# Optimization experiments

Hardware: AMD Instinct MI355X
Metric: run time of the kernel (lower is better)

## Reference

```python
import jax, jax.numpy as jnp
import numpy as np

EMBED_DIM = 512
NUM_HEADS = 8
HEAD_DIM = EMBED_DIM // NUM_HEADS


def setup_inputs() -> dict:
    key = jax.random.key(0)
    k_x, k_qkv, k_proj, k_pb = jax.random.split(key, 4)
    B, N, C = 2, 4096, EMBED_DIM
    x = jax.random.normal(k_x, (B, N, C), dtype=jnp.float32)
    # nn.Linear(embed_dim, 3*embed_dim, bias=False): weight [3C, C], y = x @ W.T
    s = 1.0 / np.sqrt(C)
    w_qkv = jax.random.uniform(k_qkv, (3 * C, C), dtype=jnp.float32, minval=-s, maxval=s)
    w_proj = jax.random.uniform(k_proj, (C, C), dtype=jnp.float32, minval=-s, maxval=s)
    b_proj = jax.random.uniform(k_pb, (C,), dtype=jnp.float32, minval=-s, maxval=s)
    return {"x": x, "w_qkv": w_qkv, "w_proj": w_proj, "b_proj": b_proj}


def reference(x, w_qkv, w_proj, b_proj):
    B, N, C = x.shape
    H, D = NUM_HEADS, HEAD_DIM
    scale = D ** -0.5
    qkv = jnp.einsum('bnc,fc->bnf', x, w_qkv)           # [B, N, 3C]
    qkv = qkv.reshape(B, N, 3, H, D)
    q, k, v = [jnp.transpose(qkv[:, :, i], (0, 2, 1, 3)) for i in range(3)]  # [B,H,N,D]
    attn = jnp.einsum('bhnd,bhmd->bhnm', q, k) * scale  # [B,H,N,N]
    # additive causal mask: -inf above the diagonal
    causal = jnp.triu(jnp.full((N, N), -jnp.inf, dtype=attn.dtype), k=1)
    attn = jax.nn.softmax(attn + causal, axis=-1)
    out = jnp.einsum('bhnm,bhmd->bhnd', attn, v)        # [B,H,N,D]
    out = jnp.transpose(out, (0, 2, 1, 3)).reshape(B, N, C)
    return jnp.einsum('bnc,oc->bno', out, w_proj) + b_proj
```

## Files before the change

kernel.cpp:

```cpp
#include <hip/hip_runtime.h>
#include <hip/hip_bf16.h>


typedef __attribute__((ext_vector_type(8))) short s16x8;
typedef __attribute__((ext_vector_type(4))) float f32x4;

#define QSCALE 0.18033688011112042f

__device__ __forceinline__ ushort f2bf(float f) {
  unsigned u = __float_as_uint(f);
  u = (u + 0x7FFFu + ((u >> 16) & 1u)) >> 16;
  return (ushort)u;
}

__device__ __forceinline__ unsigned cvt_pk_bf16(float a, float b) {
  unsigned r;
  asm("v_cvt_pk_bf16_f32 %0, %1, %2" : "=v"(r) : "v"(a), "v"(b));
  return r;
}

__device__ __forceinline__ float bflo(unsigned u) { return __uint_as_float(u << 16); }
__device__ __forceinline__ float bfhi(unsigned u) { return __uint_as_float(u & 0xffff0000u); }

__global__ __launch_bounds__(256) void cvt_all(const float* __restrict__ x,
                                               const float* __restrict__ wq,
                                               const float* __restrict__ wp,
                                               ushort* __restrict__ xb,
                                               ushort* __restrict__ wqb,
                                               ushort* __restrict__ wpb) {
  int i = blockIdx.x * 256 + threadIdx.x;
  const float* src;
  ushort* dst;
  int off;
  if (i < 1048576) {
    src = x; dst = xb; off = i;
  } else if (i < 1245184) {
    src = wq; dst = wqb; off = i - 1048576;
  } else {
    src = wp; dst = wpb; off = i - 1245184;
  }
  float4 v = reinterpret_cast<const float4*>(src)[off];
  ushort4 o;
  o.x = f2bf(v.x); o.y = f2bf(v.y); o.z = f2bf(v.z); o.w = f2bf(v.w);
  reinterpret_cast<ushort4*>(dst)[off] = o;
}

template <int EPI>
__global__ __launch_bounds__(256) void gemm_bt(const ushort* __restrict__ A,
                                               const ushort* __restrict__ W,
                                               ushort* __restrict__ q_ws,
                                               ushort* __restrict__ k_ws,
                                               ushort* __restrict__ vt_ws,
                                               float* __restrict__ outf,
                                               const float* __restrict__ bias) {
  __shared__ ushort As[128 * 32];
  __shared__ ushort Bs[128 * 32];
  const int tid = threadIdx.x;
  const int lane = tid & 63, wv = tid >> 6;
  const int wm = wv >> 1, wn = wv & 1;
  const int l15 = lane & 15, g = lane >> 4;
  const int tm = blockIdx.y * 128, tn = blockIdx.x * 128;

  f32x4 acc[4][4] = {};

  for (int k0 = 0; k0 < 512; k0 += 32) {
#pragma unroll
    for (int it = 0; it < 2; ++it) {
      int slot = it * 256 + tid;
      int row = slot >> 2;
      int ch = (slot & 3) ^ ((row >> 1) & 3);
      const int sb = (it * 256 + wv * 64) * 8;
      __builtin_amdgcn_global_load_lds(
          (const __attribute__((address_space(1))) void*)(A + (size_t)(tm + row) * 512 + k0 +
                                                          ch * 8),
          (__attribute__((address_space(3))) void*)(As + sb), 16, 0, 0);
      __builtin_amdgcn_global_load_lds(
          (const __attribute__((address_space(1))) void*)(W + (size_t)(tn + row) * 512 + k0 +
                                                          ch * 8),
          (__attribute__((address_space(3))) void*)(Bs + sb), 16, 0, 0);
    }
    __syncthreads();
    s16x8 af[4], bfr[4];
#pragma unroll
    for (int i = 0; i < 4; ++i) {
      int Ra = wm * 64 + i * 16 + l15;
      af[i] = reinterpret_cast<const s16x8*>(As)[Ra * 4 + (g ^ ((Ra >> 1) & 3))];
      int Rb = wn * 64 + i * 16 + l15;
      bfr[i] = reinterpret_cast<const s16x8*>(Bs)[Rb * 4 + (g ^ ((Rb >> 1) & 3))];
    }
#pragma unroll
    for (int mi = 0; mi < 4; ++mi)
#pragma unroll
      for (int ni = 0; ni < 4; ++ni)
        acc[mi][ni] =
            __builtin_amdgcn_mfma_f32_16x16x32_bf16(af[mi], bfr[ni], acc[mi][ni], 0, 0, 0);
    __syncthreads();
  }

  const int rowb = tm + wm * 64 + g * 4;
  const int colb = tn + wn * 64 + l15;
#pragma unroll
  for (int mi = 0; mi < 4; ++mi) {
#pragma unroll
    for (int ni = 0; ni < 4; ++ni) {
      int r0 = rowb + mi * 16;
      int col = colb + ni * 16;
      if (EPI == 0) {
        int i3 = col >> 9, h = (col >> 6) & 7, d = col & 63;
        int b = r0 >> 12;
        int bh = b * 8 + h;
        if (i3 == 2) {
          int n0 = r0 & 4095;
          int kt = n0 >> 6, ce = (n0 >> 5) & 1, ge = (n0 >> 3) & 3, je = n0 & 7;
          int nbe = d >> 4, le = d & 15;
          ushort4 pk;
          pk.x = f2bf(acc[mi][ni][0]);
          pk.y = f2bf(acc[mi][ni][1]);
          pk.z = f2bf(acc[mi][ni][2]);
          pk.w = f2bf(acc[mi][ni][3]);
          *reinterpret_cast<ushort4*>(
              vt_ws + (((size_t)bh * 64 + kt) * 8 + nbe * 2 + ce) * 512 + (ge * 16 + le) * 8 +
              je) = pk;
        } else if (i3 == 1) {
          int ce = d >> 5, ge = (d >> 3) & 3, je = d & 7;
#pragma unroll
          for (int r = 0; r < 4; ++r) {
            int n = (r0 + r) & 4095;
            int kt = n >> 6, le = n & 15, nbe = (n >> 4) & 3;
            k_ws[(((size_t)bh * 64 + kt) * 8 + nbe * 2 + ce) * 512 + (ge * 16 + le) * 8 + je] =
                f2bf(acc[mi][ni][r]);
          }
        } else {
          int n0 = r0 & 4095;
#pragma unroll
          for (int r = 0; r < 4; ++r)
            q_ws[((size_t)bh * 4096 + (n0 + r)) * 64 + d] = f2bf(acc[mi][ni][r] * QSCALE);
        }
      } else {
#pragma unroll
        for (int r = 0; r < 4; ++r)
          outf[(size_t)(r0 + r) * 512 + col] = acc[mi][ni][r] + bias[col];
      }
    }
  }
}

__global__ __launch_bounds__(64, 2) void attn_kernel(const ushort* __restrict__ Q,
                                                     const ushort* __restrict__ Kk,
                                                     const ushort* __restrict__ Vt,
                                                     ushort* __restrict__ O,
                                                     ushort* __restrict__ po,
                                                     float* __restrict__ ml) {
  __shared__ ushort P_lds[32 * 64];
  const int lane = threadIdx.x & 63;
  const int l15 = lane & 15, g = lane >> 4;
  const int L = blockIdx.x;
  const int p = L & 7, j2 = L >> 3;
  const int bh = p * 2 + (j2 & 1);
  const int i = j2 >> 1;
  const int r = i / 3;
  const int kind = i - r * 3;
  int qt, klo, khi, half = 0;
  bool partial;
  if (kind == 2) {
    qt = 63 - r;
    partial = false;
    klo = 0;
    khi = qt >> 1;
  } else {
    qt = 127 - r;
    partial = true;
    half = kind;
    const int ktm = qt >> 1;
    const int mid = (ktm + 2) >> 1;
    klo = kind ? mid : 0;
    khi = kind ? ktm : (mid - 1);
  }
  const int ktmax = qt >> 1;
  const int qw = qt * 32;
  const size_t baseQ = (size_t)bh * 4096 * 64;

  s16x8 aq[2][2];
#pragma unroll
  for (int s = 0; s < 2; ++s) {
    const ushort* qp = Q + baseQ + (size_t)(qw + s * 16 + l15) * 64 + g * 8;
    aq[s][0] = *reinterpret_cast<const s16x8*>(qp);
    aq[s][1] = *reinterpret_cast<const s16x8*>(qp + 32);
  }

  f32x4 o[2][4] = {};
  float m[2] = {-1e30f, -1e30f};
  float l[2] = {0.f, 0.f};
  const int swz = (l15 & 7) << 3;
  const ushort* kb = Kk + ((size_t)bh * 64) * 4096 + lane * 8;
  const ushort* vb = Vt + ((size_t)bh * 64) * 4096 + lane * 8;

  s16x8 kfA[8], kfB[8];
#pragma unroll
  for (int t = 0; t < 8; ++t)
    kfA[t] = *reinterpret_cast<const s16x8*>(kb + (size_t)klo * 4096 + t * 512);

#define ATTN_STEP(KC, KN, KT)                                                             \
  do {                                                                                    \
    const ushort* vp = vb + (size_t)(KT) * 4096;                                          \
    s16x8 vf[8];                                                                          \
    _Pragma("unroll") for (int t = 0; t < 8; ++t)                                         \
        vf[t] = *reinterpret_cast<const s16x8*>(vp + t * 512);                            \
    const int knx = ((KT) >= khi) ? khi : ((KT) + 1);                                     \
    const ushort* kpn = kb + (size_t)knx * 4096;                                          \
    _Pragma("unroll") for (int t = 0; t < 8; ++t)                                         \
        KN[t] = *reinterpret_cast<const s16x8*>(kpn + t * 512);                           \
    f32x4 st[2][4] = {};                                                                  \
    __builtin_amdgcn_s_setprio(1);                                                        \
    _Pragma("unroll") for (int nb = 0; nb < 4; ++nb) {                                    \
      _Pragma("unroll") for (int s = 0; s < 2; ++s) {                                     \
        st[s][nb] = __builtin_amdgcn_mfma_f32_16x16x32_bf16(KC[nb * 2 + 0], aq[s][0],     \
                                                            st[s][nb], 0, 0, 0);         \
        st[s][nb] = __builtin_amdgcn_mfma_f32_16x16x32_bf16(KC[nb * 2 + 1], aq[s][1],     \
                                                            st[s][nb], 0, 0, 0);         \
      }                                                                                   \
    }                                                                                     \
    __builtin_amdgcn_s_setprio(0);                                                        \
    if ((KT) == ktmax) {                                  \
      const int k0d = (KT) * 64;                                                          \
      _Pragma("unroll") for (int s = 0; s < 2; ++s)                                       \
          _Pragma("unroll") for (int nb = 0; nb < 4; ++nb)                                \
              _Pragma("unroll") for (int r2 = 0; r2 < 4; ++r2)                            \
                  if (k0d + nb * 16 + g * 4 + r2 > qw + s * 16 + l15)                     \
                    st[s][nb][r2] = -1e30f;                                               \
    }                                                                                     \
    _Pragma("unroll") for (int s = 0; s < 2; ++s) {                                       \
      float a0 = fmaxf(fmaxf(st[s][0][0], st[s][0][1]), fmaxf(st[s][0][2], st[s][0][3])); \
      float a1 = fmaxf(fmaxf(st[s][1][0], st[s][1][1]), fmaxf(st[s][1][2], st[s][1][3])); \
      float a2 = fmaxf(fmaxf(st[s][2][0], st[s][2][1]), fmaxf(st[s][2][2], st[s][2][3])); \
      float a3 = fmaxf(fmaxf(st[s][3][0], st[s][3][1]), fmaxf(st[s][3][2], st[s][3][3])); \
      float pm = fmaxf(fmaxf(a0, a1), fmaxf(a2, a3));                 \
      if (!__all(pm - m[s] <= 8.0f)) {                   \
        float pmf = fmaxf(pm, __shfl_xor(pm, 16));                                        \
        pmf = fmaxf(pmf, __shfl_xor(pmf, 32));                                            \
        const float mn = fmaxf(m[s], pmf);                                                \
        const float al = __builtin_amdgcn_exp2f(m[s] - mn);                               \
        l[s] *= al;                                                                       \
        m[s] = mn;                                                                        \
        _Pragma("unroll") for (int nb = 0; nb < 4; ++nb)                                  \
            _Pragma("unroll") for (int r2 = 0; r2 < 4; ++r2) o[s][nb][r2] *= al;          \
      }                                                                                   \
      float rs = 0.f;                                                                     \
      _Pragma("unroll") for (int nb = 0; nb < 4; ++nb) {                                  \
        float p0 = __builtin_amdgcn_exp2f(st[s][nb][0] - m[s]);                           \
        float p1 = __builtin_amdgcn_exp2f(st[s][nb][1] - m[s]);                           \
        float p2 = __builtin_amdgcn_exp2f(st[s][nb][2] - m[s]);                           \
        float p3 = __builtin_amdgcn_exp2f(st[s][nb][3] - m[s]);                           \
        rs += (p0 + p1) + (p2 + p3);                                                      \
        uint2 w;                                                                          \
        w.x = cvt_pk_bf16(p0, p1);                                                        \
        w.y = cvt_pk_bf16(p2, p3);                                                        \
        *reinterpret_cast<uint2*>(P_lds + (s * 16 + l15) * 64 +                           \
                                  ((nb * 16 + g * 4) ^ swz)) = w;                         \
      }                                                                                   \
      l[s] += rs;                                                                         \
    }                                                                                     \
    s16x8 pa[2][2];                                                                       \
    _Pragma("unroll") for (int s = 0; s < 2; ++s)                                         \
        _Pragma("unroll") for (int c = 0; c < 2; ++c)                                     \
            pa[s][c] = *reinterpret_cast<const s16x8*>(P_lds + (s * 16 + l15) * 64 +      \
                                                       ((c * 32 + g * 8) ^ swz));         \
    __builtin_amdgcn_s_setprio(1);                                                        \
    _Pragma("unroll") for (int nb = 0; nb < 4; ++nb) {                                    \
      _Pragma("unroll") for (int s = 0; s < 2; ++s) {                                     \
        o[s][nb] = __builtin_amdgcn_mfma_f32_16x16x32_bf16(vf[nb * 2 + 0], pa[s][0],      \
                                                           o[s][nb], 0, 0, 0);            \
        o[s][nb] = __builtin_amdgcn_mfma_f32_16x16x32_bf16(vf[nb * 2 + 1], pa[s][1],      \
                                                           o[s][nb], 0, 0, 0);            \
      }                                                                                   \
    }                                                                                     \
    __builtin_amdgcn_s_setprio(0);                                                        \
  } while (0)

  int kt = klo;
  for (;;) {
    ATTN_STEP(kfA, kfB, kt);
    if (++kt > khi) break;
    ATTN_STEP(kfB, kfA, kt);
    if (++kt > khi) break;
  }
#undef ATTN_STEP

  float lr[2];
#pragma unroll
  for (int s = 0; s < 2; ++s) {
    float ls = l[s];
    ls += __shfl_xor(ls, 16);
    ls += __shfl_xor(ls, 32);
    lr[s] = ls;
  }

  if (!partial) {
    const int b = bh >> 3, h = bh & 7;
#pragma unroll
    for (int s = 0; s < 2; ++s) {
      const float linv = 1.0f / lr[s];
      const size_t rowo = (size_t)(b * 4096 + qw + s * 16 + l15) * 512 + h * 64;
#pragma unroll
      for (int nb = 0; nb < 4; ++nb) {
        uint2 pk;
        pk.x = cvt_pk_bf16(o[s][nb][0] * linv, o[s][nb][1] * linv);
        pk.y = cvt_pk_bf16(o[s][nb][2] * linv, o[s][nb][3] * linv);
        *reinterpret_cast<uint2*>(&O[rowo + nb * 16 + g * 4]) = pk;
      }
    }
  } else {
    const int t2 = (bh * 64 + (qt - 64)) * 2 + half;
#pragma unroll
    for (int s = 0; s < 2; ++s) {
      const float linv = 1.0f / lr[s];
      const int row = s * 16 + l15;
      const size_t pbase = ((size_t)t2 * 32 + row) * 64;
#pragma unroll
      for (int nb = 0; nb < 4; ++nb) {
        uint2 pk;
        pk.x = cvt_pk_bf16(o[s][nb][0] * linv, o[s][nb][1] * linv);
        pk.y = cvt_pk_bf16(o[s][nb][2] * linv, o[s][nb][3] * linv);
        *reinterpret_cast<uint2*>(po + pbase + nb * 16 + g * 4) = pk;
      }
      if (g == 0) {
        float2 v;
        v.x = m[s];
        v.y = lr[s];
        *reinterpret_cast<float2*>(ml + ((size_t)t2 * 32 + row) * 2) = v;
      }
    }
  }
}

__global__ __launch_bounds__(64) void attn_merge(const ushort* __restrict__ po,
                                                 const float* __restrict__ ml,
                                                 ushort* __restrict__ O) {
  const int L = blockIdx.x, tid = threadIdx.x;
  const int p = L & 7, q2 = L >> 3;
  const int bh = p * 2 + (q2 & 1);
  const int qt = 64 + (q2 >> 1);
  const int t = bh * 64 + (qt - 64);
  const int row = tid >> 1, dh = (tid & 1) * 32;
  const float2 ml0 = *reinterpret_cast<const float2*>(ml + ((size_t)(t * 2 + 0) * 32 + row) * 2);
  const float2 ml1 = *reinterpret_cast<const float2*>(ml + ((size_t)(t * 2 + 1) * 32 + row) * 2);
  const float ms = fmaxf(ml0.x, ml1.x);
  const float w0 = __builtin_amdgcn_exp2f(ml0.x - ms) * ml0.y;
  const float w1 = __builtin_amdgcn_exp2f(ml1.x - ms) * ml1.y;
  const float inv = 1.0f / (w0 + w1);
  const float c0 = w0 * inv, c1 = w1 * inv;
  const int b = bh >> 3, h = bh & 7;
  const size_t rowo = (size_t)(b * 4096 + qt * 32 + row) * 512 + h * 64 + dh;
  const ushort* p0 = po + ((size_t)(t * 2 + 0) * 32 + row) * 64 + dh;
  const ushort* p1 = po + ((size_t)(t * 2 + 1) * 32 + row) * 64 + dh;
#pragma unroll
  for (int j = 0; j < 4; ++j) {
    uint4 a = reinterpret_cast<const uint4*>(p0)[j];
    uint4 bb = reinterpret_cast<const uint4*>(p1)[j];
    uint4 out;
    out.x = cvt_pk_bf16(c0 * bflo(a.x) + c1 * bflo(bb.x), c0 * bfhi(a.x) + c1 * bfhi(bb.x));
    out.y = cvt_pk_bf16(c0 * bflo(a.y) + c1 * bflo(bb.y), c0 * bfhi(a.y) + c1 * bfhi(bb.y));
    out.z = cvt_pk_bf16(c0 * bflo(a.z) + c1 * bflo(bb.z), c0 * bfhi(a.z) + c1 * bfhi(bb.z));
    out.w = cvt_pk_bf16(c0 * bflo(a.w) + c1 * bflo(bb.w), c0 * bfhi(a.w) + c1 * bfhi(bb.w));
    reinterpret_cast<uint4*>(&O[rowo])[j] = out;
  }
}

extern "C" void kernel_launch(void* const* d_in, const int* in_sizes, int n_in,
                              void* d_out, int out_size, void* d_ws, size_t ws_size,
                              hipStream_t stream) {
  const float* x = (const float*)d_in[0];
  const float* w_qkv = (const float*)d_in[1];
  const float* w_proj = (const float*)d_in[2];
  const float* b_proj = (const float*)d_in[3];
  float* out = (float*)d_out;

  ushort* xb = (ushort*)d_ws;
  ushort* wqkvb = xb + (size_t)8192 * 512;
  ushort* wprojb = wqkvb + (size_t)1536 * 512;
  ushort* qws = wprojb + (size_t)512 * 512;
  ushort* kws = qws + (size_t)16 * 4096 * 64;
  ushort* vtws = kws + (size_t)16 * 4096 * 64;
  ushort* ows = vtws + (size_t)16 * 4096 * 64;

  cvt_all<<<5120, 256, 0, stream>>>(x, w_qkv, w_proj, xb, wqkvb, wprojb);

  gemm_bt<0><<<dim3(12, 64), 256, 0, stream>>>(xb, wqkvb, qws, kws, vtws, nullptr, nullptr);

  ushort* po = xb;
  float* ml = (float*)wqkvb;

  attn_kernel<<<3072, 64, 0, stream>>>(qws, kws, vtws, ows, po, ml);
  attn_merge<<<1024, 64, 0, stream>>>(po, ml, ows);

  gemm_bt<1><<<dim3(4, 64), 256, 0, stream>>>(ows, wprojb, nullptr, nullptr, nullptr, out,
                                              b_proj);
}
```

Measured before the change: 116.2 us.

## Shrink attention query tile to 16 rows and double the block count

Each single-wave attention block now handles 16 query rows instead of 32. The grid, the causal split schedule and the partial-merge indexing are rescaled so the number of blocks doubles, and launch bounds now ask for 3 waves per SIMD. The goal is more parallelism and occupancy through fewer registers per wave. In exchange, every K/V tile is loaded from memory twice as often per query row, since each loaded tile now feeds half as many MFMAs.

```diff
diff --git a/kernel.cpp b/kernel.cpp
--- a/kernel.cpp
+++ b/kernel.cpp
@@ -145,13 +145,13 @@
   }
 }
 
-__global__ __launch_bounds__(64, 2) void attn_kernel(const ushort* __restrict__ Q,
+__global__ __launch_bounds__(64, 3) void attn_kernel(const ushort* __restrict__ Q,
                                                      const ushort* __restrict__ Kk,
                                                      const ushort* __restrict__ Vt,
                                                      ushort* __restrict__ O,
                                                      ushort* __restrict__ po,
                                                      float* __restrict__ ml) {
-  __shared__ ushort P_lds[32 * 64];
+  __shared__ ushort P_lds[16 * 64];
   const int lane = threadIdx.x & 63;
   const int l15 = lane & 15, g = lane >> 4;
   const int L = blockIdx.x;
@@ -163,34 +163,33 @@
   int qt, klo, khi, half = 0;
   bool partial;
   if (kind == 2) {
-    qt = 63 - r;
+    qt = 127 - r;
     partial = false;
     klo = 0;
-    khi = qt >> 1;
+    khi = qt >> 2;
   } else {
-    qt = 127 - r;
+    qt = 255 - r;
     partial = true;
     half = kind;
-    const int ktm = qt >> 1;
+    const int ktm = qt >> 2;
     const int mid = (ktm + 2) >> 1;
     klo = kind ? mid : 0;
     khi = kind ? ktm : (mid - 1);
   }
-  const int ktmax = qt >> 1;
-  const int qw = qt * 32;
+  const int ktmax = qt >> 2;
+  const int qw = qt * 16;
   const size_t baseQ = (size_t)bh * 4096 * 64;
 
-  s16x8 aq[2][2];
-#pragma unroll
-  for (int s = 0; s < 2; ++s) {
-    const ushort* qp = Q + baseQ + (size_t)(qw + s * 16 + l15) * 64 + g * 8;
-    aq[s][0] = *reinterpret_cast<const s16x8*>(qp);
-    aq[s][1] = *reinterpret_cast<const s16x8*>(qp + 32);
-  }
-
-  f32x4 o[2][4] = {};
-  float m[2] = {-1e30f, -1e30f};
-  float l[2] = {0.f, 0.f};
+  s16x8 aq0, aq1;
+  {
+    const ushort* qp = Q + baseQ + (size_t)(qw + l15) * 64 + g * 8;
+    aq0 = *reinterpret_cast<const s16x8*>(qp);
+    aq1 = *reinterpret_cast<const s16x8*>(qp + 32);
+  }
+
+  f32x4 o[4] = {};
+  float m = -1e30f;
+  float l = 0.f;
   const int swz = (l15 & 7) << 3;
   const ushort* kb = Kk + ((size_t)bh * 64) * 4096 + lane * 8;
   const ushort* vb = Vt + ((size_t)bh * 64) * 4096 + lane * 8;
@@ -210,69 +209,61 @@
     const ushort* kpn = kb + (size_t)knx * 4096;                                          \
     _Pragma("unroll") for (int t = 0; t < 8; ++t)                                         \
         KN[t] = *reinterpret_cast<const s16x8*>(kpn + t * 512);                           \
-    f32x4 st[2][4] = {};                                                                  \
+    f32x4 st[4] = {};                                                                     \
     __builtin_amdgcn_s_setprio(1);                                                        \
     _Pragma("unroll") for (int nb = 0; nb < 4; ++nb) {                                    \
-      _Pragma("unroll") for (int s = 0; s < 2; ++s) {                                     \
-        st[s][nb] = __builtin_amdgcn_mfma_f32_16x16x32_bf16(KC[nb * 2 + 0], aq[s][0],     \
-                                                            st[s][nb], 0, 0, 0);         \
-        st[s][nb] = __builtin_amdgcn_mfma_f32_16x16x32_bf16(KC[nb * 2 + 1], aq[s][1],     \
-                                                            st[s][nb], 0, 0, 0);         \
-      }                                                                                   \
+      st[nb] = __builtin_amdgcn_mfma_f32_16x16x32_bf16(KC[nb * 2 + 0], aq0, st[nb],       \
+                                                       0, 0, 0);                          \
+      st[nb] = __builtin_amdgcn_mfma_f32_16x16x32_bf16(KC[nb * 2 + 1], aq1, st[nb],       \
+                                                       0, 0, 0);                          \
     }                                                                                     \
     __builtin_amdgcn_s_setprio(0);                                                        \
     if ((KT) == ktmax) {                                  \
       const int k0d = (KT) * 64;                                                          \
-      _Pragma("unroll") for (int s = 0; s < 2; ++s)                                       \
-          _Pragma("unroll") for (int nb = 0; nb < 4; ++nb)                                \
-              _Pragma("unroll") for (int r2 = 0; r2 < 4; ++r2)                            \
-                  if (k0d + nb * 16 + g * 4 + r2 > qw + s * 16 + l15)                     \
-                    st[s][nb][r2] = -1e30f;                                               \
+      _Pragma("unroll") for (int nb = 0; nb < 4; ++nb)                                    \
+          _Pragma("unroll") for (int r2 = 0; r2 < 4; ++r2)                                \
+              if (k0d + nb * 16 + g * 4 + r2 > qw + l15) st[nb][r2] = -1e30f;             \
     }                                                                                     \
-    _Pragma("unroll") for (int s = 0; s < 2; ++s) {                                       \
-      float a0 = fmaxf(fmaxf(st[s][0][0], st[s][0][1]), fmaxf(st[s][0][2], st[s][0][3])); \
-      float a1 = fmaxf(fmaxf(st[s][1][0], st[s][1][1]), fmaxf(st[s][1][2], st[s][1][3])); \
-      float a2 = fmaxf(fmaxf(st[s][2][0], st[s][2][1]), fmaxf(st[s][2][2], st[s][2][3])); \
-      float a3 = fmaxf(fmaxf(st[s][3][0], st[s][3][1]), fmaxf(st[s][3][2], st[s][3][3])); \
+    {                                                                                     \
+      float a0 = fmaxf(fmaxf(st[0][0], st[0][1]), fmaxf(st[0][2], st[0][3]));             \
+      float a1 = fmaxf(fmaxf(st[1][0], st[1][1]), fmaxf(st[1][2], st[1][3]));             \
+      float a2 = fmaxf(fmaxf(st[2][0], st[2][1]), fmaxf(st[2][2], st[2][3]));             \
+      float a3 = fmaxf(fmaxf(st[3][0], st[3][1]), fmaxf(st[3][2], st[3][3]));             \
       float pm = fmaxf(fmaxf(a0, a1), fmaxf(a2, a3));                 \
-      if (!__all(pm - m[s] <= 8.0f)) {                   \
+      if (!__all(pm - m <= 8.0f)) {                      \
         float pmf = fmaxf(pm, __shfl_xor(pm, 16));                                        \
         pmf = fmaxf(pmf, __shfl_xor(pmf, 32));                                            \
-        const float mn = fmaxf(m[s], pmf);                                                \
-        const float al = __builtin_amdgcn_exp2f(m[s] - mn);                               \
-        l[s] *= al;                                                                       \
-        m[s] = mn;                                                                        \
+        const float mn = fmaxf(m, pmf);                                                   \
+        const float al = __builtin_amdgcn_exp2f(m - mn);                                  \
+        l *= al;                                                                          \
+        m = mn;                                                                           \
         _Pragma("unroll") for (int nb = 0; nb < 4; ++nb)                                  \
-            _Pragma("unroll") for (int r2 = 0; r2 < 4; ++r2) o[s][nb][r2] *= al;          \
+            _Pragma("unroll") for (int r2 = 0; r2 < 4; ++r2) o[nb][r2] *= al;             \
       }                                                                                   \
       float rs = 0.f;                                                                     \
       _Pragma("unroll") for (int nb = 0; nb < 4; ++nb) {                                  \
-        float p0 = __builtin_amdgcn_exp2f(st[s][nb][0] - m[s]);                           \
-        float p1 = __builtin_amdgcn_exp2f(st[s][nb][1] - m[s]);                           \
-        float p2 = __builtin_amdgcn_exp2f(st[s][nb][2] - m[s]);                           \
-        float p3 = __builtin_amdgcn_exp2f(st[s][nb][3] - m[s]);                           \
+        float p0 = __builtin_amdgcn_exp2f(st[nb][0] - m);                                 \
+        float p1 = __builtin_amdgcn_exp2f(st[nb][1] - m);                                 \
+        float p2 = __builtin_amdgcn_exp2f(st[nb][2] - m);                                 \
+        float p3 = __builtin_amdgcn_exp2f(st[nb][3] - m);                                 \
         rs += (p0 + p1) + (p2 + p3);                                                      \
         uint2 w;                                                                          \
         w.x = cvt_pk_bf16(p0, p1);                                                        \
         w.y = cvt_pk_bf16(p2, p3);                                                        \
-        *reinterpret_cast<uint2*>(P_lds + (s * 16 + l15) * 64 +                           \
-                                  ((nb * 16 + g * 4) ^ swz)) = w;                         \
+        *reinterpret_cast<uint2*>(P_lds + l15 * 64 + ((nb * 16 + g * 4) ^ swz)) = w;      \
       }                                                                                   \
-      l[s] += rs;                                                                         \
+      l += rs;                                                                            \
     }                                                                                     \
-    s16x8 pa[2][2];                                                                       \
-    _Pragma("unroll") for (int s = 0; s < 2; ++s)                                         \
-        _Pragma("unroll") for (int c = 0; c < 2; ++c)                                     \
-            pa[s][c] = *reinterpret_cast<const s16x8*>(P_lds + (s * 16 + l15) * 64 +      \
-                                                       ((c * 32 + g * 8) ^ swz));         \
+    s16x8 pa[2];                                                                          \
+    _Pragma("unroll") for (int c = 0; c < 2; ++c)                                         \
+        pa[c] = *reinterpret_cast<const s16x8*>(P_lds + l15 * 64 +                        \
+                                                ((c * 32 + g * 8) ^ swz));                \
     __builtin_amdgcn_s_setprio(1);                                                        \
     _Pragma("unroll") for (int nb = 0; nb < 4; ++nb) {                                    \
-      _Pragma("unroll") for (int s = 0; s < 2; ++s) {                                     \
-        o[s][nb] = __builtin_amdgcn_mfma_f32_16x16x32_bf16(vf[nb * 2 + 0], pa[s][0],      \
-                                                           o[s][nb], 0, 0, 0);            \
-        o[s][nb] = __builtin_amdgcn_mfma_f32_16x16x32_bf16(vf[nb * 2 + 1], pa[s][1],      \
-                                                           o[s][nb], 0, 0, 0);            \
-      }                                                                                   \
+      o[nb] = __builtin_amdgcn_mfma_f32_16x16x32_bf16(vf[nb * 2 + 0], pa[0], o[nb],       \
+                                                      0, 0, 0);                           \
+      o[nb] = __builtin_amdgcn_mfma_f32_16x16x32_bf16(vf[nb * 2 + 1], pa[1], o[nb],       \
+                                                      0, 0, 0);                           \
     }                                                                                     \
     __builtin_amdgcn_s_setprio(0);                                                        \
   } while (0)
@@ -286,49 +277,37 @@
   }
 #undef ATTN_STEP
 
-  float lr[2];
-#pragma unroll
-  for (int s = 0; s < 2; ++s) {
-    float ls = l[s];
-    ls += __shfl_xor(ls, 16);
-    ls += __shfl_xor(ls, 32);
-    lr[s] = ls;
-  }
+  float lr = l;
+  lr += __shfl_xor(lr, 16);
+  lr += __shfl_xor(lr, 32);
 
   if (!partial) {
     const int b = bh >> 3, h = bh & 7;
-#pragma unroll
-    for (int s = 0; s < 2; ++s) {
-      const float linv = 1.0f / lr[s];
-      const size_t rowo = (size_t)(b * 4096 + qw + s * 16 + l15) * 512 + h * 64;
-#pragma unroll
-      for (int nb = 0; nb < 4; ++nb) {
-        uint2 pk;
-        pk.x = cvt_pk_bf16(o[s][nb][0] * linv, o[s][nb][1] * linv);
-        pk.y = cvt_pk_bf16(o[s][nb][2] * linv, o[s][nb][3] * linv);
-        *reinterpret_cast<uint2*>(&O[rowo + nb * 16 + g * 4]) = pk;
-      }
+    const float linv = 1.0f / lr;
+    const size_t rowo = (size_t)(b * 4096 + qw + l15) * 512 + h * 64;
+#pragma unroll
+    for (int nb = 0; nb < 4; ++nb) {
+      uint2 pk;
+      pk.x = cvt_pk_bf16(o[nb][0] * linv, o[nb][1] * linv);
+      pk.y = cvt_pk_bf16(o[nb][2] * linv, o[nb][3] * linv);
+      *reinterpret_cast<uint2*>(&O[rowo + nb * 16 + g * 4]) = pk;
     }
   } else {
-    const int t2 = (bh * 64 + (qt - 64)) * 2 + half;
-#pragma unroll
-    for (int s = 0; s < 2; ++s) {
-      const float linv = 1.0f / lr[s];
-      const int row = s * 16 + l15;
-      const size_t pbase = ((size_t)t2 * 32 + row) * 64;
-#pragma unroll
-      for (int nb = 0; nb < 4; ++nb) {
-        uint2 pk;
-        pk.x = cvt_pk_bf16(o[s][nb][0] * linv, o[s][nb][1] * linv);
-        pk.y = cvt_pk_bf16(o[s][nb][2] * linv, o[s][nb][3] * linv);
-        *reinterpret_cast<uint2*>(po + pbase + nb * 16 + g * 4) = pk;
-      }
-      if (g == 0) {
-        float2 v;
-        v.x = m[s];
-        v.y = lr[s];
-        *reinterpret_cast<float2*>(ml + ((size_t)t2 * 32 + row) * 2) = v;
-      }
+    const int t2 = (bh * 128 + (qt - 128)) * 2 + half;
+    const float linv = 1.0f / lr;
+    const size_t pbase = ((size_t)t2 * 16 + l15) * 64;
+#pragma unroll
+    for (int nb = 0; nb < 4; ++nb) {
+      uint2 pk;
+      pk.x = cvt_pk_bf16(o[nb][0] * linv, o[nb][1] * linv);
+      pk.y = cvt_pk_bf16(o[nb][2] * linv, o[nb][3] * linv);
+      *reinterpret_cast<uint2*>(po + pbase + nb * 16 + g * 4) = pk;
+    }
+    if (g == 0) {
+      float2 v;
+      v.x = m;
+      v.y = lr;
+      *reinterpret_cast<float2*>(ml + ((size_t)t2 * 16 + l15) * 2) = v;
     }
   }
 }
@@ -336,25 +315,25 @@
 __global__ __launch_bounds__(64) void attn_merge(const ushort* __restrict__ po,
                                                  const float* __restrict__ ml,
                                                  ushort* __restrict__ O) {
-  const int L = blockIdx.x, tid = threadIdx.x;
-  const int p = L & 7, q2 = L >> 3;
+  const int M = blockIdx.x, tid = threadIdx.x;
+  const int p = M & 7, q2 = M >> 3;
   const int bh = p * 2 + (q2 & 1);
-  const int qt = 64 + (q2 >> 1);
-  const int t = bh * 64 + (qt - 64);
-  const int row = tid >> 1, dh = (tid & 1) * 32;
-  const float2 ml0 = *reinterpret_cast<const float2*>(ml + ((size_t)(t * 2 + 0) * 32 + row) * 2);
-  const float2 ml1 = *reinterpret_cast<const float2*>(ml + ((size_t)(t * 2 + 1) * 32 + row) * 2);
+  const int qt = 128 + (q2 >> 1);
+  const int t = bh * 128 + (qt - 128);
+  const int row = tid & 15, seg = tid >> 4;
+  const float2 ml0 = *reinterpret_cast<const float2*>(ml + ((size_t)(t * 2 + 0) * 16 + row) * 2);
+  const float2 ml1 = *reinterpret_cast<const float2*>(ml + ((size_t)(t * 2 + 1) * 16 + row) * 2);
   const float ms = fmaxf(ml0.x, ml1.x);
   const float w0 = __builtin_amdgcn_exp2f(ml0.x - ms) * ml0.y;
   const float w1 = __builtin_amdgcn_exp2f(ml1.x - ms) * ml1.y;
   const float inv = 1.0f / (w0 + w1);
   const float c0 = w0 * inv, c1 = w1 * inv;
   const int b = bh >> 3, h = bh & 7;
-  const size_t rowo = (size_t)(b * 4096 + qt * 32 + row) * 512 + h * 64 + dh;
-  const ushort* p0 = po + ((size_t)(t * 2 + 0) * 32 + row) * 64 + dh;
-  const ushort* p1 = po + ((size_t)(t * 2 + 1) * 32 + row) * 64 + dh;
-#pragma unroll
-  for (int j = 0; j < 4; ++j) {
+  const size_t rowo = (size_t)(b * 4096 + qt * 16 + row) * 512 + h * 64 + seg * 16;
+  const ushort* p0 = po + ((size_t)(t * 2 + 0) * 16 + row) * 64 + seg * 16;
+  const ushort* p1 = po + ((size_t)(t * 2 + 1) * 16 + row) * 64 + seg * 16;
+#pragma unroll
+  for (int j = 0; j < 2; ++j) {
     uint4 a = reinterpret_cast<const uint4*>(p0)[j];
     uint4 bb = reinterpret_cast<const uint4*>(p1)[j];
     uint4 out;
@@ -390,8 +369,8 @@
   ushort* po = xb;
   float* ml = (float*)wqkvb;
 
-  attn_kernel<<<3072, 64, 0, stream>>>(qws, kws, vtws, ows, po, ml);
-  attn_merge<<<1024, 64, 0, stream>>>(po, ml, ows);
+  attn_kernel<<<6144, 64, 0, stream>>>(qws, kws, vtws, ows, po, ml);
+  attn_merge<<<2048, 64, 0, stream>>>(po, ml, ows);
 
   gemm_bt<1><<<dim3(4, 64), 256, 0, stream>>>(ows, wprojb, nullptr, nullptr, nullptr, out,
                                               b_proj);
```

Measured after the change: 130.2 us. 1.12x slower.
